# Kernel tuning notes

Hardware: AMD Instinct MI355X
Metric: run time of the kernel (lower is better)

Reference implementation:

```python
import jax, jax.numpy as jnp
import numpy as np

N_NODES = 156
NFEAT = 256
NHID = 128
B = 16384
T = 24
HLSTM = 32
ALPHA = 0.2


def setup_inputs() -> dict:
    key = jax.random.key(0)
    ks = jax.random.split(key, 16)
    f32 = jnp.float32
    inp = {
        "embedding": jax.random.normal(ks[0], (N_NODES, NFEAT), f32),
        "x": jax.random.normal(ks[1], (B, T, N_NODES), f32),
        "adj": jax.random.randint(ks[2], (N_NODES, N_NODES), 0, 2, jnp.int32),
        # GAT params (xavier-ish scale)
        "W_recent": jax.random.normal(ks[3], (NFEAT, NHID), f32) * 0.08,
        "a_recent": jax.random.normal(ks[4], (2 * NHID, 1), f32) * 0.1,
        "W_period": jax.random.normal(ks[5], (NFEAT, NHID), f32) * 0.08,
        "a_period": jax.random.normal(ks[6], (2 * NHID, 1), f32) * 0.1,
        # LSTM params, torch layout: weight_ih [4H, D], weight_hh [4H, H]
        "Wih_r": jax.random.normal(ks[7], (4 * HLSTM, N_NODES), f32) * 0.08,
        "Whh_r": jax.random.normal(ks[8], (4 * HLSTM, HLSTM), f32) * 0.08,
        "bih_r": jnp.zeros((4 * HLSTM,), f32),
        "bhh_r": jnp.zeros((4 * HLSTM,), f32),
        "Wih_p": jax.random.normal(ks[9], (4 * HLSTM, N_NODES), f32) * 0.08,
        "Whh_p": jax.random.normal(ks[10], (4 * HLSTM, HLSTM), f32) * 0.08,
        "bih_p": jnp.zeros((4 * HLSTM,), f32),
        "bhh_p": jnp.zeros((4 * HLSTM,), f32),
        "fc_W": jax.random.normal(ks[11], (N_NODES, 2 * HLSTM), f32) * 0.1,
        "fc_b": jnp.zeros((N_NODES,), f32),
    }
    return inp


def _gat_attention(embedding, W, a, adj):
    # h = embedding @ W : [N, F]
    h = embedding @ W
    F = h.shape[1]
    # e[i,j] = leakyrelu(h_i . a[:F] + h_j . a[F:])  (same math as the
    # repeat/cat construction, without materializing [N*N, 2F])
    s1 = h @ a[:F, 0]   # [N]
    s2 = h @ a[F:, 0]   # [N]
    e = jax.nn.leaky_relu(s1[:, None] + s2[None, :], ALPHA)
    e = jnp.where(adj > 0, e, jnp.float32(-9e15))
    return jax.nn.softmax(e, axis=1)  # [N, N]


def _lstm_last(x_seq, Wih, Whh, bih, bhh):
    # x_seq: [B, T, D]; returns last hidden state [B, H]
    H = Whh.shape[1]
    Bn = x_seq.shape[0]
    h0 = jnp.zeros((Bn, H), x_seq.dtype)
    c0 = jnp.zeros((Bn, H), x_seq.dtype)
    bias = bih + bhh

    def step(carry, xt):
        h, c = carry
        g = xt @ Wih.T + h @ Whh.T + bias
        i, f, gg, o = jnp.split(g, 4, axis=-1)  # torch gate order i,f,g,o
        c = jax.nn.sigmoid(f) * c + jax.nn.sigmoid(i) * jnp.tanh(gg)
        h = jax.nn.sigmoid(o) * jnp.tanh(c)
        return (h, c), None

    (h, c), _ = jax.lax.scan(step, (h0, c0), jnp.swapaxes(x_seq, 0, 1))
    return h


def reference(embedding, x, adj, W_recent, a_recent, W_period, a_period,
              Wih_r, Whh_r, bih_r, bhh_r, Wih_p, Whh_p, bih_p, bhh_p,
              fc_W, fc_b):
    recent = x[:, :4, :]   # [B, 4, N]
    period = x[:, 4:, :]   # [B, T-4, N]

    # attention depends only on embedding/adj -> identical across timesteps
    attn_r = _gat_attention(embedding, W_recent, a_recent, adj)  # [N, N]
    attn_p = _gat_attention(embedding, W_period, a_period, adj)

    # out[b,t,i] = sum_j attn[i,j] * x[b,t,j]
    xr = jnp.einsum('ij,btj->bti', attn_r, recent)
    xp = jnp.einsum('ij,btj->bti', attn_p, period)

    hr = _lstm_last(xr, Wih_r, Whh_r, bih_r, bhh_r)  # [B, 32]
    hp = _lstm_last(xp, Wih_p, Whh_p, bih_p, bhh_p)  # [B, 32]

    h = jnp.concatenate([hr, hp], axis=1)            # [B, 64]
    return h @ fc_W.T + fc_b                         # [B, 156]
```

## Files before the change

kernel.cpp:

```cpp
#include <hip/hip_runtime.h>
#include <hip/hip_bf16.h>
#include <math.h>

#define N_NODES 156
#define NFEAT 256
#define NHID 128
#define BATCH 16384
#define TT 24
#define HLSTM 32
#define G4 128
#define ALPHA 0.2f
#define NW 2
#define ROWS_B (NW*16)
#define XSTRIDE (TT*N_NODES)
#define SLOTF 2560

typedef __attribute__((ext_vector_type(8))) short bf16x8;
typedef __attribute__((ext_vector_type(4))) float f32x4;

static __device__ __forceinline__ unsigned short f2bf(float f) {
    unsigned u = __float_as_uint(f);
    u += 0x7fffu + ((u >> 16) & 1u);
    return (unsigned short)(u >> 16);
}
static __device__ __forceinline__ bf16x8 cv8(float4 a, float4 b) {
    union { __hip_bfloat16 h[8]; bf16x8 v; } u;
    u.h[0] = __float2bfloat16(a.x); u.h[1] = __float2bfloat16(a.y);
    u.h[2] = __float2bfloat16(a.z); u.h[3] = __float2bfloat16(a.w);
    u.h[4] = __float2bfloat16(b.x); u.h[5] = __float2bfloat16(b.y);
    u.h[6] = __float2bfloat16(b.z); u.h[7] = __float2bfloat16(b.w);
    return u.v;
}
static __device__ __forceinline__ float sigm(float x) { return 1.f / (1.f + __expf(-x)); }
static __device__ __forceinline__ float tanh_(float x) { return 1.f - 2.f / (__expf(2.f * x) + 1.f); }

__global__ void k_gat_s(const float* __restrict__ emb,
                        const float* __restrict__ Wr, const float* __restrict__ ar,
                        const float* __restrict__ Wp, const float* __restrict__ ap,
                        float* __restrict__ s_buf ) {
    int i = blockIdx.x;
    int gat = blockIdx.y;
    const float* W = gat ? Wp : Wr;
    const float* a = gat ? ap : ar;
    int j = threadIdx.x;
    __shared__ float erow[NFEAT];
    __shared__ float red[128];
    for (int k = j; k < NFEAT; k += 128) erow[k] = emb[i*NFEAT + k];
    __syncthreads();
    float h = 0.f;
    for (int k = 0; k < NFEAT; ++k) h = fmaf(erow[k], W[k*NHID + j], h);
    float v1 = h * a[j];
    float v2 = h * a[NHID + j];
    red[j] = v1; __syncthreads();
    for (int s = 64; s > 0; s >>= 1) { if (j < s) red[j] += red[j+s]; __syncthreads(); }
    if (j == 0) s_buf[(gat*2+0)*N_NODES + i] = red[0];
    __syncthreads();
    red[j] = v2; __syncthreads();
    for (int s = 64; s > 0; s >>= 1) { if (j < s) red[j] += red[j+s]; __syncthreads(); }
    if (j == 0) s_buf[(gat*2+1)*N_NODES + i] = red[0];
}

__global__ void k_attn(const float* __restrict__ s_buf, const int* __restrict__ adj,
                       float* __restrict__ attn ) {
    int i = blockIdx.x, gat = blockIdx.y;
    int j = threadIdx.x;
    __shared__ float red[256];
    float s1 = s_buf[(gat*2+0)*N_NODES + i];
    bool act = (j < N_NODES);
    float e = -INFINITY;
    if (act) {
        float s2 = s_buf[(gat*2+1)*N_NODES + j];
        float z = s1 + s2;
        z = (z > 0.f) ? z : ALPHA * z;
        if (adj[i*N_NODES + j] <= 0) z = -9e15f;
        e = z;
    }
    red[j] = e; __syncthreads();
    for (int s = 128; s > 0; s >>= 1) { if (j < s) red[j] = fmaxf(red[j], red[j+s]); __syncthreads(); }
    float m = red[0]; __syncthreads();
    float val = act ? __expf(e - m) : 0.f;
    red[j] = val; __syncthreads();
    for (int s = 128; s > 0; s >>= 1) { if (j < s) red[j] += red[j+s]; __syncthreads(); }
    float inv = 1.f / red[0];
    if (act) attn[(gat*N_NODES + i)*N_NODES + j] = val * inv;
}

__global__ void k_prep(const float* __restrict__ attn,
                       const float* __restrict__ Wih_r, const float* __restrict__ Wih_p,
                       const float* __restrict__ Whh_r, const float* __restrict__ Whh_p,
                       const float* __restrict__ bih_r, const float* __restrict__ bhh_r,
                       const float* __restrict__ bih_p, const float* __restrict__ bhh_p,
                       unsigned short* __restrict__ Mbf ,
                       unsigned short* __restrict__ Whhbf ,
                       float* __restrict__ bias2 ) {
    int g = blockIdx.x, gat = blockIdx.y;
    const float* Wih = gat ? Wih_p : Wih_r;
    const float* A = attn + gat*N_NODES*N_NODES;
    int j = threadIdx.x;
    if (j < 160) {
        float acc = 0.f;
        if (j < N_NODES)
            for (int n = 0; n < N_NODES; ++n)
                acc = fmaf(Wih[g*N_NODES + n], A[n*N_NODES + j], acc);
        Mbf[(gat*G4 + g)*160 + j] = f2bf(acc);
    }
    if (j < HLSTM)
        Whhbf[(gat*G4 + g)*HLSTM + j] = f2bf((gat ? Whh_p : Whh_r)[g*HLSTM + j]);
    if (g == 0 && j < G4)
        bias2[gat*G4 + j] = gat ? (bih_p[j] + bhh_p[j]) : (bih_r[j] + bhh_r[j]);
}

__global__ void __launch_bounds__(NW*64, 1)
k_fused(const float* __restrict__ x,
        const unsigned short* __restrict__ Mbf,
        const unsigned short* __restrict__ Whhbf,
        const float* __restrict__ bias2,
        const float* __restrict__ fcW,
        const float* __restrict__ fcb,
        float* __restrict__ out) {
    __shared__ __align__(16) float xsf[NW][3][SLOTF];
    __shared__ __align__(16) unsigned short hfrag[NW*512];
    __shared__ __align__(16) unsigned short hcatf[NW*1024];

    const int tid = threadIdx.x;
    const int w  = tid >> 6;
    const int l  = tid & 63;
    const int lm = l & 15;
    const int lg = l >> 4;
    const int b0 = blockIdx.x * ROWS_B;

    unsigned goff[10];
    #pragma unroll
    for (int i = 0; i < 10; ++i) {
        int c = l + i*64;
        int r = c / 39;
        int cf = (c - r*39) * 4;
        if (r > 15) r = 15;
        goff[i] = (unsigned)(r*XSTRIDE + cf);
    }
    const float* xg = x + (size_t)(b0 + 16*w) * XSTRIDE;

    bf16x8 bfr[8][5];
    bf16x8 wrec[8];
    float  bias_v[8];
    float  cst[8];
    const float4 f4z = make_float4(0.f, 0.f, 0.f, 0.f);

#define LOAD_FRAGS(Mb, Wb, bs) do {                                          \
    _Pragma("unroll")                                                        \
    for (int nt = 0; nt < 8; ++nt) {                                         \
        int n_ = nt*16 + lm;                                                 \
        _Pragma("unroll")                                                    \
        for (int kf = 0; kf < 5; ++kf)                                       \
            bfr[nt][kf] = *(const bf16x8*)((Mb) + n_*160 + kf*32 + lg*8);    \
        wrec[nt]   = *(const bf16x8*)((Wb) + n_*HLSTM + lg*8);               \
        bias_v[nt] = (bs)[n_];                                               \
    } } while (0)

    #pragma unroll
    for (int ds = 0; ds < 2; ++ds)
        #pragma unroll
        for (int i = 0; i < 4; ++i) {
            hfrag[w*512 + ((lm>>3) + 2*ds)*128 + (lg*4 + i)*8 + (lm&7)] = 0;
            cst[ds*4 + i] = 0.f;
        }
    LOAD_FRAGS(Mbf, Whhbf, bias2);

#define DMA_STEP(S_, T_) do {                                                 \
    const float* gp_ = xg + (T_)*N_NODES;                                     \
    _Pragma("unroll")                                                         \
    for (int i_ = 0; i_ < 10; ++i_)                                           \
        __builtin_amdgcn_global_load_lds(                                     \
            (const __attribute__((address_space(1))) void*)(gp_ + goff[i_]),  \
            (__attribute__((address_space(3))) void*)(&xsf[w][S_][i_*256]),   \
            16, 0, 0);                                                        \
    } while (0)

#define WAITVM(N_) asm volatile("s_waitcnt vmcnt(" #N_ ")" ::: "memory")

#define STEP(S_, T_, ISS_, TN_) do {                                          \
    const float* xr_ = &xsf[w][S_][0] + lm*N_NODES + lg*8;                    \
    float4 q0_[5], q1_[5];                                                    \
    _Pragma("unroll")                                                         \
    for (int kf = 0; kf < 5; ++kf) {                                          \
        q0_[kf] = *(const float4*)(xr_ + kf*32);                              \
        q1_[kf] = *(const float4*)(xr_ + kf*32 + 4);                          \
    }                                                                         \
    bf16x8 hf_ = *(const bf16x8*)(hfrag + w*512 + l*8);                       \
    if (lg == 3) q1_[4] = f4z;                       \
    bf16x8 af_[5];                                                            \
    _Pragma("unroll")                                                         \
    for (int kf = 0; kf < 5; ++kf) af_[kf] = cv8(q0_[kf], q1_[kf]);           \
    asm volatile("s_waitcnt lgkmcnt(0)" ::: "memory");                        \
    __builtin_amdgcn_sched_barrier(0);                                        \
    if (ISS_) DMA_STEP(S_, TN_);                \
    f32x4 acc[8];                                                             \
    _Pragma("unroll")                                                         \
    for (int nt = 0; nt < 8; ++nt)                                            \
        acc[nt] = (f32x4){bias_v[nt], bias_v[nt], bias_v[nt], bias_v[nt]};    \
    _Pragma("unroll")                                                         \
    for (int kf = 0; kf < 5; ++kf)                                            \
        _Pragma("unroll")                                                     \
        for (int nt = 0; nt < 8; ++nt)                                        \
            acc[nt] = __builtin_amdgcn_mfma_f32_16x16x32_bf16(af_[kf], bfr[nt][kf], acc[nt], 0, 0, 0); \
    _Pragma("unroll")                                                         \
    for (int nt = 0; nt < 8; ++nt)                                            \
        acc[nt] = __builtin_amdgcn_mfma_f32_16x16x32_bf16(hf_, wrec[nt], acc[nt], 0, 0, 0); \
    _Pragma("unroll")                                                         \
    for (int ds = 0; ds < 2; ++ds)                                            \
        _Pragma("unroll")                                                     \
        for (int i = 0; i < 4; ++i) {                                         \
            float si = sigm(acc[0 + ds][i]);                                  \
            float sf = sigm(acc[2 + ds][i]);                                  \
            float tg = tanh_(acc[4 + ds][i]);                                 \
            float so = sigm(acc[6 + ds][i]);                                  \
            float c  = sf * cst[ds*4 + i] + si * tg;                          \
            float h  = so * tanh_(c);                                         \
            int cidx = ((lm>>3) + 2*ds)*128 + (lg*4 + i)*8 + (lm&7);          \
            if ((T_) == 3) {                \
                hcatf[w*1024 + cidx] = f2bf(h);                               \
                hfrag[w*512 + cidx]  = 0;                                     \
                cst[ds*4 + i] = 0.f;                                          \
            } else {                                                          \
                cst[ds*4 + i] = c;                                            \
                hfrag[w*512 + cidx] = f2bf(h);                                \
                if ((T_) == TT-1) hcatf[w*1024 + 512 + cidx] = f2bf(h);       \
            }                                                                 \
        }                                                                     \
    if ((T_) == 3) LOAD_FRAGS(Mbf + G4*160, Whhbf + G4*HLSTM, bias2 + G4);    \
    } while (0)

    DMA_STEP(0, 0);
    DMA_STEP(1, 1);
    DMA_STEP(2, 2);

    int s = 0;
    #pragma unroll 3
    for (int t = 0; t < TT-2; ++t) {
        WAITVM(20);
        STEP(s, t, (t < TT-3), t+3);
        s = (s == 2) ? 0 : s + 1;
    }
    WAITVM(10);
    STEP(1, TT-2, 0, 0);
    WAITVM(0);
    STEP(2, TT-1, 0, 0);

    {
        bf16x8 ha0 = *(const bf16x8*)(hcatf + w*1024 + l*8);
        bf16x8 ha1 = *(const bf16x8*)(hcatf + w*1024 + 512 + l*8);
        #pragma unroll
        for (int nt = 0; nt < 10; ++nt) {
            int n  = nt*16 + lm;
            int nc = n < 155 ? n : 155;
            const float* wp0 = fcW + nc*64 + lg*8;
            const float* wp1 = fcW + nc*64 + 32 + lg*8;
            bf16x8 wf0 = cv8(*(const float4*)wp0, *(const float4*)(wp0 + 4));
            bf16x8 wf1 = cv8(*(const float4*)wp1, *(const float4*)(wp1 + 4));
            f32x4 fa = (f32x4){0.f, 0.f, 0.f, 0.f};
            fa = __builtin_amdgcn_mfma_f32_16x16x32_bf16(ha0, wf0, fa, 0, 0, 0);
            fa = __builtin_amdgcn_mfma_f32_16x16x32_bf16(ha1, wf1, fa, 0, 0, 0);
            if (n < N_NODES) {
                float bn = fcb[n];
                #pragma unroll
                for (int i = 0; i < 4; ++i)
                    out[(size_t)(b0 + 16*w + lg*4 + i)*N_NODES + n] = fa[i] + bn;
            }
        }
    }
#undef STEP
#undef WAITVM
#undef DMA_STEP
#undef LOAD_FRAGS
}

extern "C" void kernel_launch(void* const* d_in, const int* in_sizes, int n_in,
                              void* d_out, int out_size, void* d_ws, size_t ws_size,
                              hipStream_t stream) {
    (void)in_sizes; (void)n_in; (void)out_size; (void)ws_size;
    const float* emb   = (const float*)d_in[0];
    const float* x     = (const float*)d_in[1];
    const int*   adj   = (const int*)d_in[2];
    const float* Wr    = (const float*)d_in[3];
    const float* ar    = (const float*)d_in[4];
    const float* Wp    = (const float*)d_in[5];
    const float* ap    = (const float*)d_in[6];
    const float* Wih_r = (const float*)d_in[7];
    const float* Whh_r = (const float*)d_in[8];
    const float* bih_r = (const float*)d_in[9];
    const float* bhh_r = (const float*)d_in[10];
    const float* Wih_p = (const float*)d_in[11];
    const float* Whh_p = (const float*)d_in[12];
    const float* bih_p = (const float*)d_in[13];
    const float* bhh_p = (const float*)d_in[14];
    const float* fcW   = (const float*)d_in[15];
    const float* fcb   = (const float*)d_in[16];
    float* out = (float*)d_out;

    char* ws = (char*)d_ws;
    size_t off = 0;
    auto alloc = [&](size_t bytes) {
        char* p = ws + off;
        off += (bytes + 255) & ~(size_t)255;
        return p;
    };
    float*          attn  = (float*)alloc(2*156*156*sizeof(float));
    float*          sbuf  = (float*)alloc(4*156*sizeof(float));
    unsigned short* Mbf   = (unsigned short*)alloc(2*G4*160*sizeof(unsigned short));
    unsigned short* Whhbf = (unsigned short*)alloc(2*G4*HLSTM*sizeof(unsigned short));
    float*          bias2 = (float*)alloc(2*G4*sizeof(float));

    k_gat_s<<<dim3(156, 2), 128, 0, stream>>>(emb, Wr, ar, Wp, ap, sbuf);
    k_attn<<<dim3(156, 2), 256, 0, stream>>>(sbuf, adj, attn);
    k_prep<<<dim3(128, 2), 192, 0, stream>>>(attn, Wih_r, Wih_p, Whh_r, Whh_p,
                                             bih_r, bhh_r, bih_p, bhh_p,
                                             Mbf, Whhbf, bias2);
    k_fused<<<dim3(BATCH/ROWS_B), NW*64, 0, stream>>>(x, Mbf, Whhbf, bias2, fcW, fcb, out);
}
```

Baseline: 94.19 us.

## Deepen x prefetch to four LDS slots, issuing DMA in timestep pairs

The triple-buffered per-timestep LDS prefetch becomes a four-slot ring. Async global-to-LDS loads are now issued for two timesteps at once, every other step, and the last partial chunk is trimmed so no redundant rows are fetched. The hcatf shared buffer is dropped: the recent-branch hidden state is kept in registers and the final hidden state is read back from hfrag, with the fc stage reusing the x buffer. This raises the number of loads in flight and cuts per-step issue overhead, at the cost of more LDS for x and a tighter vmcnt schedule that must match the paired loads.

```diff
diff --git a/kernel.cpp b/kernel.cpp
--- a/kernel.cpp
+++ b/kernel.cpp
@@ -13,7 +13,7 @@
 #define NW 2
 #define ROWS_B (NW*16)
 #define XSTRIDE (TT*N_NODES)
-#define SLOTF 2560
+#define SLOTF 2496
 
 typedef __attribute__((ext_vector_type(8))) short bf16x8;
 typedef __attribute__((ext_vector_type(4))) float f32x4;
@@ -118,9 +118,8 @@
         const float* __restrict__ fcW,
         const float* __restrict__ fcb,
         float* __restrict__ out) {
-    __shared__ __align__(16) float xsf[NW][3][SLOTF];
+    __shared__ __align__(16) float xsf[NW][4][SLOTF];
     __shared__ __align__(16) unsigned short hfrag[NW*512];
-    __shared__ __align__(16) unsigned short hcatf[NW*1024];
 
     const int tid = threadIdx.x;
     const int w  = tid >> 6;
@@ -133,9 +132,9 @@
     #pragma unroll
     for (int i = 0; i < 10; ++i) {
         int c = l + i*64;
+        if (c > 623) c = 623;
         int r = c / 39;
         int cf = (c - r*39) * 4;
-        if (r > 15) r = 15;
         goff[i] = (unsigned)(r*XSTRIDE + cf);
     }
     const float* xg = x + (size_t)(b0 + 16*w) * XSTRIDE;
@@ -144,6 +143,7 @@
     bf16x8 wrec[8];
     float  bias_v[8];
     float  cst[8];
+    unsigned short hrv[8];
     const float4 f4z = make_float4(0.f, 0.f, 0.f, 0.f);
 
 #define LOAD_FRAGS(Mb, Wb, bs) do {                                          \
@@ -166,20 +166,27 @@
         }
     LOAD_FRAGS(Mbf, Whhbf, bias2);
 
-#define DMA_STEP(S_, T_) do {                                                 \
-    const float* gp_ = xg + (T_)*N_NODES;                                     \
-    _Pragma("unroll")                                                         \
-    for (int i_ = 0; i_ < 10; ++i_)                                           \
-        __builtin_amdgcn_global_load_lds(                                     \
-            (const __attribute__((address_space(1))) void*)(gp_ + goff[i_]),  \
-            (__attribute__((address_space(3))) void*)(&xsf[w][S_][i_*256]),   \
-            16, 0, 0);                                                        \
-    } while (0)
+#define DMA_PAIR(TA, TB) do {                                                 \
+    const float* pa_ = xg + (size_t)(TA)*N_NODES;                             \
+    const float* pb_ = xg + (size_t)(TB)*N_NODES;                             \
+    float* da_ = &xsf[w][(TA)&3][0];                                          \
+    float* db_ = &xsf[w][(TB)&3][0];                                          \
+    _Pragma("unroll")                                                         \
+    for (int i_ = 0; i_ < 10; ++i_) {                                         \
+        if (i_ < 9 || l < 48) {                                               \
+            __builtin_amdgcn_global_load_lds(                                 \
+                (const __attribute__((address_space(1))) void*)(pa_ + goff[i_]), \
+                (__attribute__((address_space(3))) void*)(da_ + i_*256), 16, 0, 0); \
+            __builtin_amdgcn_global_load_lds(                                 \
+                (const __attribute__((address_space(1))) void*)(pb_ + goff[i_]), \
+                (__attribute__((address_space(3))) void*)(db_ + i_*256), 16, 0, 0); \
+        }                                                                     \
+    } } while (0)
 
 #define WAITVM(N_) asm volatile("s_waitcnt vmcnt(" #N_ ")" ::: "memory")
 
-#define STEP(S_, T_, ISS_, TN_) do {                                          \
-    const float* xr_ = &xsf[w][S_][0] + lm*N_NODES + lg*8;                    \
+#define STEP(T_, ISS_) do {                                                   \
+    const float* xr_ = &xsf[w][(T_)&3][0] + lm*N_NODES + lg*8;                \
     float4 q0_[5], q1_[5];                                                    \
     _Pragma("unroll")                                                         \
     for (int kf = 0; kf < 5; ++kf) {                                          \
@@ -193,7 +200,7 @@
     for (int kf = 0; kf < 5; ++kf) af_[kf] = cv8(q0_[kf], q1_[kf]);           \
     asm volatile("s_waitcnt lgkmcnt(0)" ::: "memory");                        \
     __builtin_amdgcn_sched_barrier(0);                                        \
-    if (ISS_) DMA_STEP(S_, TN_);                \
+    if (ISS_) DMA_PAIR((T_)+3, (T_)+4);      \
     f32x4 acc[8];                                                             \
     _Pragma("unroll")                                                         \
     for (int nt = 0; nt < 8; ++nt)                                            \
@@ -218,37 +225,43 @@
             float h  = so * tanh_(c);                                         \
             int cidx = ((lm>>3) + 2*ds)*128 + (lg*4 + i)*8 + (lm&7);          \
             if ((T_) == 3) {                \
-                hcatf[w*1024 + cidx] = f2bf(h);                               \
+                hrv[ds*4 + i] = f2bf(h);                                      \
                 hfrag[w*512 + cidx]  = 0;                                     \
                 cst[ds*4 + i] = 0.f;                                          \
             } else {                                                          \
                 cst[ds*4 + i] = c;                                            \
                 hfrag[w*512 + cidx] = f2bf(h);                                \
-                if ((T_) == TT-1) hcatf[w*1024 + 512 + cidx] = f2bf(h);       \
             }                                                                 \
         }                                                                     \
     if ((T_) == 3) LOAD_FRAGS(Mbf + G4*160, Whhbf + G4*HLSTM, bias2 + G4);    \
     } while (0)
 
-    DMA_STEP(0, 0);
-    DMA_STEP(1, 1);
-    DMA_STEP(2, 2);
-
-    int s = 0;
-    #pragma unroll 3
-    for (int t = 0; t < TT-2; ++t) {
+    DMA_PAIR(0, 1);
+    DMA_PAIR(2, 3);
+
+    for (int p = 0; p < 11; ++p) {
+        int t0 = 2*p;
         WAITVM(20);
-        STEP(s, t, (t < TT-3), t+3);
-        s = (s == 2) ? 0 : s + 1;
-    }
-    WAITVM(10);
-    STEP(1, TT-2, 0, 0);
+        STEP(t0, 0);
+        STEP(t0 + 1, (p < 10));
+    }
     WAITVM(0);
-    STEP(2, TT-1, 0, 0);
+    STEP(22, 0);
+    STEP(23, 0);
 
     {
-        bf16x8 ha0 = *(const bf16x8*)(hcatf + w*1024 + l*8);
-        bf16x8 ha1 = *(const bf16x8*)(hcatf + w*1024 + 512 + l*8);
+        unsigned short* hrA = (unsigned short*)&xsf[w][0][0];
+        #pragma unroll
+        for (int ds = 0; ds < 2; ++ds)
+            #pragma unroll
+            for (int i = 0; i < 4; ++i) {
+                int cidx = ((lm>>3) + 2*ds)*128 + (lg*4 + i)*8 + (lm&7);
+                hrA[cidx] = hrv[ds*4 + i];
+            }
+        asm volatile("s_waitcnt lgkmcnt(0)" ::: "memory");
+        __builtin_amdgcn_sched_barrier(0);
+        bf16x8 ha0 = *(const bf16x8*)(hrA + l*8);
+        bf16x8 ha1 = *(const bf16x8*)(hfrag + w*512 + l*8);
         #pragma unroll
         for (int nt = 0; nt < 10; ++nt) {
             int n  = nt*16 + lm;
@@ -270,7 +283,7 @@
     }
 #undef STEP
 #undef WAITVM
-#undef DMA_STEP
+#undef DMA_PAIR
 #undef LOAD_FRAGS
 }
 
```

Result: no change. 95.46 us (+1.3%).

## Split LSTM gate columns across two waves per 16-row block

Applied to the files above, without the earlier changes.

Each block now handles 16 batch rows with two waves that split the 128 gate columns, instead of each wave owning 16 rows with all gates. Wave 0 computes the input-gate times candidate product and passes it through LDS; wave 1 finishes the cell and hidden update. The x tile DMA is shared across both waves, and the grid doubles to 1024 blocks with launch bounds allowing two blocks per CU. This halves per-wave MFMA work and register pressure to raise occupancy and shorten the serial recurrence per wave. The cost is two block barriers per timestep and an LDS exchange.

```diff
diff --git a/kernel.cpp b/kernel.cpp
--- a/kernel.cpp
+++ b/kernel.cpp
@@ -10,10 +10,8 @@
 #define HLSTM 32
 #define G4 128
 #define ALPHA 0.2f
-#define NW 2
-#define ROWS_B (NW*16)
 #define XSTRIDE (TT*N_NODES)
-#define SLOTF 2560
+#define SLOTF 2496
 
 typedef __attribute__((ext_vector_type(8))) short bf16x8;
 typedef __attribute__((ext_vector_type(4))) float f32x4;
@@ -110,7 +108,7 @@
         bias2[gat*G4 + j] = gat ? (bih_p[j] + bhh_p[j]) : (bih_r[j] + bhh_r[j]);
 }
 
-__global__ void __launch_bounds__(NW*64, 1)
+__global__ void __launch_bounds__(128, 2)
 k_fused(const float* __restrict__ x,
         const unsigned short* __restrict__ Mbf,
         const unsigned short* __restrict__ Whhbf,
@@ -118,38 +116,41 @@
         const float* __restrict__ fcW,
         const float* __restrict__ fcb,
         float* __restrict__ out) {
-    __shared__ __align__(16) float xsf[NW][3][SLOTF];
-    __shared__ __align__(16) unsigned short hfrag[NW*512];
-    __shared__ __align__(16) unsigned short hcatf[NW*1024];
+    __shared__ __align__(16) float xsf[3][SLOTF];
+    __shared__ __align__(16) unsigned short hfrag[512];
+    __shared__ __align__(16) float P_ls[512];
+    __shared__ __align__(16) unsigned short hcat[16*72];
 
     const int tid = threadIdx.x;
     const int w  = tid >> 6;
     const int l  = tid & 63;
     const int lm = l & 15;
     const int lg = l >> 4;
-    const int b0 = blockIdx.x * ROWS_B;
-
-    unsigned goff[10];
+    const int b0 = blockIdx.x * 16;
+    const float* xg = x + (size_t)b0 * XSTRIDE;
+
+    unsigned goff[5];
     #pragma unroll
-    for (int i = 0; i < 10; ++i) {
-        int c = l + i*64;
+    for (int k = 0; k < 5; ++k) {
+        int c = l + (w*5 + k)*64;
+        if (c > 623) c = 623;
         int r = c / 39;
-        int cf = (c - r*39) * 4;
-        if (r > 15) r = 15;
-        goff[i] = (unsigned)(r*XSTRIDE + cf);
-    }
-    const float* xg = x + (size_t)(b0 + 16*w) * XSTRIDE;
-
-    bf16x8 bfr[8][5];
-    bf16x8 wrec[8];
-    float  bias_v[8];
+        goff[k] = (unsigned)(r*XSTRIDE + (c - r*39)*4);
+    }
+
+    bf16x8 bfr[4][5];
+    bf16x8 wrec[4];
+    float  bias_v[4];
     float  cst[8];
+    unsigned short hrv[8], hpv[8];
+    const int nbase = w ? 2 : 0;
     const float4 f4z = make_float4(0.f, 0.f, 0.f, 0.f);
 
 #define LOAD_FRAGS(Mb, Wb, bs) do {                                          \
     _Pragma("unroll")                                                        \
-    for (int nt = 0; nt < 8; ++nt) {                                         \
-        int n_ = nt*16 + lm;                                                 \
+    for (int nt = 0; nt < 4; ++nt) {                                         \
+        int ntid = nbase + (nt & 1) + ((nt >> 1) << 2);                      \
+        int n_ = ntid*16 + lm;                                               \
         _Pragma("unroll")                                                    \
         for (int kf = 0; kf < 5; ++kf)                                       \
             bfr[nt][kf] = *(const bf16x8*)((Mb) + n_*160 + kf*32 + lg*8);    \
@@ -157,100 +158,132 @@
         bias_v[nt] = (bs)[n_];                                               \
     } } while (0)
 
-    #pragma unroll
-    for (int ds = 0; ds < 2; ++ds)
+#define DMA_STEP(S_, T_) do {                                                 \
+    const float* gp_ = xg + (size_t)(T_)*N_NODES;                             \
+    _Pragma("unroll")                                                         \
+    for (int k_ = 0; k_ < 5; ++k_) {                                          \
+        if (w*5 + k_ != 9 || l < 48)                                          \
+            __builtin_amdgcn_global_load_lds(                                 \
+                (const __attribute__((address_space(1))) void*)(gp_ + goff[k_]), \
+                (__attribute__((address_space(3))) void*)(&xsf[S_][(w*5 + k_)*256]), \
+                16, 0, 0);                                                    \
+    } } while (0)
+
+#define WAITVM(N_) asm volatile("s_waitcnt vmcnt(" #N_ ")" ::: "memory")
+#define LGKM0()    asm volatile("s_waitcnt lgkmcnt(0)" ::: "memory")
+
+    DMA_STEP(0, 0);
+    LOAD_FRAGS(Mbf, Whhbf, bias2);
+    DMA_STEP(1, 1);
+    DMA_STEP(2, 2);
+
+    if (w == 1) {
         #pragma unroll
-        for (int i = 0; i < 4; ++i) {
-            hfrag[w*512 + ((lm>>3) + 2*ds)*128 + (lg*4 + i)*8 + (lm&7)] = 0;
-            cst[ds*4 + i] = 0.f;
-        }
-    LOAD_FRAGS(Mbf, Whhbf, bias2);
-
-#define DMA_STEP(S_, T_) do {                                                 \
-    const float* gp_ = xg + (T_)*N_NODES;                                     \
-    _Pragma("unroll")                                                         \
-    for (int i_ = 0; i_ < 10; ++i_)                                           \
-        __builtin_amdgcn_global_load_lds(                                     \
-            (const __attribute__((address_space(1))) void*)(gp_ + goff[i_]),  \
-            (__attribute__((address_space(3))) void*)(&xsf[w][S_][i_*256]),   \
-            16, 0, 0);                                                        \
-    } while (0)
-
-#define WAITVM(N_) asm volatile("s_waitcnt vmcnt(" #N_ ")" ::: "memory")
-
-#define STEP(S_, T_, ISS_, TN_) do {                                          \
-    const float* xr_ = &xsf[w][S_][0] + lm*N_NODES + lg*8;                    \
+        for (int ds = 0; ds < 2; ++ds)
+            #pragma unroll
+            for (int i = 0; i < 4; ++i) {
+                hfrag[((lm>>3) + 2*ds)*128 + (lg*4 + i)*8 + (lm&7)] = 0;
+                cst[ds*4 + i] = 0.f;
+            }
+    }
+
+#define STEP(T_, S_, ISS_) do {                                               \
+    LGKM0();                                                                  \
+    __builtin_amdgcn_s_barrier();   \
+    const float* xr_ = &xsf[S_][0] + lm*N_NODES + lg*8;                       \
     float4 q0_[5], q1_[5];                                                    \
     _Pragma("unroll")                                                         \
     for (int kf = 0; kf < 5; ++kf) {                                          \
         q0_[kf] = *(const float4*)(xr_ + kf*32);                              \
         q1_[kf] = *(const float4*)(xr_ + kf*32 + 4);                          \
     }                                                                         \
-    bf16x8 hf_ = *(const bf16x8*)(hfrag + w*512 + l*8);                       \
+    bf16x8 hf_ = *(const bf16x8*)(hfrag + l*8);                               \
     if (lg == 3) q1_[4] = f4z;                       \
     bf16x8 af_[5];                                                            \
     _Pragma("unroll")                                                         \
     for (int kf = 0; kf < 5; ++kf) af_[kf] = cv8(q0_[kf], q1_[kf]);           \
-    asm volatile("s_waitcnt lgkmcnt(0)" ::: "memory");                        \
-    __builtin_amdgcn_sched_barrier(0);                                        \
-    if (ISS_) DMA_STEP(S_, TN_);                \
-    f32x4 acc[8];                                                             \
-    _Pragma("unroll")                                                         \
-    for (int nt = 0; nt < 8; ++nt)                                            \
+    f32x4 acc[4];                                                             \
+    _Pragma("unroll")                                                         \
+    for (int nt = 0; nt < 4; ++nt)                                            \
         acc[nt] = (f32x4){bias_v[nt], bias_v[nt], bias_v[nt], bias_v[nt]};    \
     _Pragma("unroll")                                                         \
     for (int kf = 0; kf < 5; ++kf)                                            \
         _Pragma("unroll")                                                     \
-        for (int nt = 0; nt < 8; ++nt)                                        \
+        for (int nt = 0; nt < 4; ++nt)                                        \
             acc[nt] = __builtin_amdgcn_mfma_f32_16x16x32_bf16(af_[kf], bfr[nt][kf], acc[nt], 0, 0, 0); \
     _Pragma("unroll")                                                         \
-    for (int nt = 0; nt < 8; ++nt)                                            \
+    for (int nt = 0; nt < 4; ++nt)                                            \
         acc[nt] = __builtin_amdgcn_mfma_f32_16x16x32_bf16(hf_, wrec[nt], acc[nt], 0, 0, 0); \
-    _Pragma("unroll")                                                         \
-    for (int ds = 0; ds < 2; ++ds)                                            \
+    float sa_[8], sb_[8];                                                     \
+    if (w == 0) {                                                             \
         _Pragma("unroll")                                                     \
-        for (int i = 0; i < 4; ++i) {                                         \
-            float si = sigm(acc[0 + ds][i]);                                  \
-            float sf = sigm(acc[2 + ds][i]);                                  \
-            float tg = tanh_(acc[4 + ds][i]);                                 \
-            float so = sigm(acc[6 + ds][i]);                                  \
-            float c  = sf * cst[ds*4 + i] + si * tg;                          \
-            float h  = so * tanh_(c);                                         \
-            int cidx = ((lm>>3) + 2*ds)*128 + (lg*4 + i)*8 + (lm&7);          \
-            if ((T_) == 3) {                \
-                hcatf[w*1024 + cidx] = f2bf(h);                               \
-                hfrag[w*512 + cidx]  = 0;                                     \
-                cst[ds*4 + i] = 0.f;                                          \
-            } else {                                                          \
-                cst[ds*4 + i] = c;                                            \
-                hfrag[w*512 + cidx] = f2bf(h);                                \
-                if ((T_) == TT-1) hcatf[w*1024 + 512 + cidx] = f2bf(h);       \
+        for (int ds = 0; ds < 2; ++ds)                                        \
+            _Pragma("unroll")                                                 \
+            for (int i = 0; i < 4; ++i) {                                     \
+                float si = sigm(acc[ds][i]);                                  \
+                float tg = tanh_(acc[2 + ds][i]);                             \
+                P_ls[(ds*4 + i)*64 + l] = si * tg;                            \
             }                                                                 \
-        }                                                                     \
+    } else {                                                                  \
+        _Pragma("unroll")                                                     \
+        for (int ds = 0; ds < 2; ++ds)                                        \
+            _Pragma("unroll")                                                 \
+            for (int i = 0; i < 4; ++i) {                                     \
+                sa_[ds*4 + i] = sigm(acc[ds][i]);                     \
+                sb_[ds*4 + i] = sigm(acc[2 + ds][i]);                 \
+            }                                                                 \
+    }                                                                         \
+    LGKM0();                                                                  \
+    __builtin_amdgcn_s_barrier();   \
+    if (ISS_) DMA_STEP(S_, (T_) + 3);            \
+    if (w == 1) {                                                             \
+        _Pragma("unroll")                                                     \
+        for (int ds = 0; ds < 2; ++ds)                                        \
+            _Pragma("unroll")                                                 \
+            for (int i = 0; i < 4; ++i) {                                     \
+                int v = ds*4 + i;                                             \
+                float c = sa_[v]*cst[v] + P_ls[v*64 + l];                     \
+                float h = sb_[v]*tanh_(c);                                    \
+                int cidx = ((lm>>3) + 2*ds)*128 + (lg*4 + i)*8 + (lm&7);      \
+                if ((T_) == 3) {                \
+                    hrv[v] = f2bf(h); hfrag[cidx] = 0; cst[v] = 0.f;          \
+                } else if ((T_) == TT-1) {                                    \
+                    hpv[v] = f2bf(h);                                         \
+                } else {                                                      \
+                    cst[v] = c; hfrag[cidx] = f2bf(h);                        \
+                }                                                             \
+            }                                                                 \
+    }                                                                         \
     if ((T_) == 3) LOAD_FRAGS(Mbf + G4*160, Whhbf + G4*HLSTM, bias2 + G4);    \
     } while (0)
 
-    DMA_STEP(0, 0);
-    DMA_STEP(1, 1);
-    DMA_STEP(2, 2);
-
-    int s = 0;
-    #pragma unroll 3
-    for (int t = 0; t < TT-2; ++t) {
-        WAITVM(20);
-        STEP(s, t, (t < TT-3), t+3);
-        s = (s == 2) ? 0 : s + 1;
-    }
-    WAITVM(10);
-    STEP(1, TT-2, 0, 0);
-    WAITVM(0);
-    STEP(2, TT-1, 0, 0);
-
+    for (int tb = 0; tb < 21; tb += 3) {
+        WAITVM(10); STEP(tb + 0, 0, 1);
+        WAITVM(10); STEP(tb + 1, 1, 1);
+        WAITVM(10); STEP(tb + 2, 2, 1);
+    }
+    WAITVM(10); STEP(21, 0, 0);
+    WAITVM(5);  STEP(22, 1, 0);
+    WAITVM(0);  STEP(23, 2, 0);
+
+    if (w == 1) {
+        #pragma unroll
+        for (int ds = 0; ds < 2; ++ds)
+            #pragma unroll
+            for (int i = 0; i < 4; ++i) {
+                int r = lg*4 + i, d = lm + 16*ds, v = ds*4 + i;
+                hcat[r*72 + d]      = hrv[v];
+                hcat[r*72 + 32 + d] = hpv[v];
+            }
+    }
+    LGKM0();
+    __builtin_amdgcn_s_barrier();
     {
-        bf16x8 ha0 = *(const bf16x8*)(hcatf + w*1024 + l*8);
-        bf16x8 ha1 = *(const bf16x8*)(hcatf + w*1024 + 512 + l*8);
+        bf16x8 ha0 = *(const bf16x8*)(hcat + lm*72 + lg*8);
+        bf16x8 ha1 = *(const bf16x8*)(hcat + lm*72 + 32 + lg*8);
         #pragma unroll
-        for (int nt = 0; nt < 10; ++nt) {
+        for (int nt5 = 0; nt5 < 5; ++nt5) {
+            int nt = w*5 + nt5;
             int n  = nt*16 + lm;
             int nc = n < 155 ? n : 155;
             const float* wp0 = fcW + nc*64 + lg*8;
@@ -264,11 +297,12 @@
                 float bn = fcb[n];
                 #pragma unroll
                 for (int i = 0; i < 4; ++i)
-                    out[(size_t)(b0 + 16*w + lg*4 + i)*N_NODES + n] = fa[i] + bn;
+                    out[(size_t)(b0 + lg*4 + i)*N_NODES + n] = fa[i] + bn;
             }
         }
     }
 #undef STEP
+#undef LGKM0
 #undef WAITVM
 #undef DMA_STEP
 #undef LOAD_FRAGS
@@ -315,5 +349,5 @@
     k_prep<<<dim3(128, 2), 192, 0, stream>>>(attn, Wih_r, Wih_p, Whh_r, Whh_p,
                                              bih_r, bhh_r, bih_p, bhh_p,
                                              Mbf, Whhbf, bias2);
-    k_fused<<<dim3(BATCH/ROWS_B), NW*64, 0, stream>>>(x, Mbf, Whhbf, bias2, fcW, fcb, out);
-}
+    k_fused<<<dim3(BATCH/16), 128, 0, stream>>>(x, Mbf, Whhbf, bias2, fcW, fcb, out);
+}
```

Result: slower. 102.6 us (+8.9%).
